# Kernel tuning notes

Measured on AMD Instinct MI355X. Metric: run time of the kernel, lower is better.

Reference implementation:

```python
import jax, jax.numpy as jnp
import numpy as np

B, S, HID = 1, 2048, 2048
H, KV, D = 32, 8, 64          # num_heads, num_kv_heads, head_dim
N_REP = H // KV               # GQA groups = 4
FF = 8192
EPS = 1e-5
ROPE_THETA = 10000.0


def _rope_tables(seq_len, dim, dtype=jnp.float32):
    inv_freq = 1.0 / (ROPE_THETA ** (jnp.arange(0, dim, 2, dtype=jnp.float32) / dim))
    t = jnp.arange(seq_len, dtype=jnp.float32)
    freqs = jnp.outer(t, inv_freq)                 # [S, D/2]
    emb = jnp.concatenate([freqs, freqs], axis=-1) # [S, D]
    return jnp.cos(emb).astype(dtype)[None], jnp.sin(emb).astype(dtype)[None]  # [1,S,D]


def setup_inputs() -> dict:
    key = jax.random.key(0)
    ks = jax.random.split(key, 10)
    s = 0.02
    cos, sin = _rope_tables(S, D)
    return {
        "hidden_states": jax.random.normal(ks[0], (B, S, HID), jnp.float32),
        "cos": cos, "sin": sin,
        "wq": jax.random.normal(ks[1], (HID, H * D), jnp.float32) * s,
        "wk": jax.random.normal(ks[2], (HID, KV * D), jnp.float32) * s,
        "wv": jax.random.normal(ks[3], (HID, KV * D), jnp.float32) * s,
        "wo": jax.random.normal(ks[4], (H * D, HID), jnp.float32) * s,
        "w_ln1": jnp.ones((HID,), jnp.float32),
        "w_ln2": jnp.ones((HID,), jnp.float32),
        "w_gate": jax.random.normal(ks[5], (HID, FF), jnp.float32) * s,
        "w_up": jax.random.normal(ks[6], (HID, FF), jnp.float32) * s,
        "w_down": jax.random.normal(ks[7], (FF, HID), jnp.float32) * s,
    }


def _rmsnorm(x, w):
    var = jnp.mean(jnp.square(x), axis=-1, keepdims=True)
    return x * jax.lax.rsqrt(var + EPS) * w


def _rotate_half(x):
    x1, x2 = jnp.split(x, 2, axis=-1)
    return jnp.concatenate([-x2, x1], axis=-1)


def _apply_rope(q, k, cos, sin):
    # q,k: [B,H,S,D]; cos,sin: [B,S,D] -> unsqueeze head dim
    c, s = cos[:, None], sin[:, None]
    return q * c + _rotate_half(q) * s, k * c + _rotate_half(k) * s


def reference(hidden_states, cos, sin, wq, wk, wv, wo, w_ln1, w_ln2, w_gate, w_up, w_down):
    residual = hidden_states
    x = _rmsnorm(hidden_states, w_ln1)

    q = (x @ wq).reshape(B, S, H, D).transpose(0, 2, 1, 3)    # [B,H,S,D]
    k = (x @ wk).reshape(B, S, KV, D).transpose(0, 2, 1, 3)   # [B,KV,S,D]
    v = (x @ wv).reshape(B, S, KV, D).transpose(0, 2, 1, 3)
    q, k = _apply_rope(q, k, cos, sin)

    # repeat_kv (interleaved) for GQA
    k = jnp.repeat(k, N_REP, axis=1)                           # [B,H,S,D]
    v = jnp.repeat(v, N_REP, axis=1)

    scale = 1.0 / np.sqrt(D)
    scores = jnp.einsum("bhqd,bhkd->bhqk", q, k) * scale       # [B,H,S,S]
    causal = jnp.tril(jnp.ones((S, S), bool))
    scores = jnp.where(causal, scores, jnp.finfo(scores.dtype).min)
    probs = jax.nn.softmax(scores, axis=-1)
    attn = jnp.einsum("bhqk,bhkd->bhqd", probs, v)             # [B,H,S,D]
    attn = attn.transpose(0, 2, 1, 3).reshape(B, S, H * D)
    attn = attn @ wo

    h = residual + attn
    residual = h
    y = _rmsnorm(h, w_ln2)
    mlp = (jax.nn.silu(y @ w_gate) * (y @ w_up)) @ w_down
    return residual + mlp
```

## Files before the change

kernel.cpp:

```cpp
#include <hip/hip_runtime.h>
#include <hip/hip_bf16.h>
#include <cstdint>

#define S_LEN 2048
#define HIDN  2048
#define NH    32
#define NKV   8
#define HD    64
#define FFN   8192
#define QKVN  3072
#define QKVLD 3072

typedef __attribute__((ext_vector_type(4)))  float f32x4;
typedef __attribute__((ext_vector_type(16))) float f32x16;
typedef __attribute__((ext_vector_type(8)))  short short8;
typedef __attribute__((ext_vector_type(4)))  short s16x4;

__device__ __forceinline__ short f2bf(float f) {
  union { float f; uint32_t u; } v; v.f = f;
  uint32_t r = v.u + 0x7FFFu + ((v.u >> 16) & 1u);
  return (short)(r >> 16);
}
__device__ __forceinline__ float bf2f(short s) {
  union { float f; uint32_t u; } v; v.u = ((uint32_t)(uint16_t)s) << 16;
  return v.f;
}
__device__ __forceinline__ unsigned packbf2(float lo, float hi) {
  return (unsigned)(uint16_t)f2bf(lo) | ((unsigned)(uint16_t)f2bf(hi) << 16);
}

#define GLOAD_LDS16(gp, lp) \
  __builtin_amdgcn_global_load_lds((const __attribute__((address_space(1))) void*)(gp), \
                                   (__attribute__((address_space(3))) void*)(lp), 16, 0, 0)

#define BARRIER()  asm volatile("s_barrier" ::: "memory")
#define LGKM0()    asm volatile("s_waitcnt lgkmcnt(0)" ::: "memory")
#define SCHED0()   __builtin_amdgcn_sched_barrier(0)
#define VMCNT(N)   asm volatile("s_waitcnt vmcnt(%0)" :: "n"(N) : "memory")

__global__ __launch_bounds__(256) void convT_kernel(const float* __restrict__ src,
    short* __restrict__ dst, int K, int N) {
  __shared__ float t[64][65];
  const int k0 = blockIdx.x * 64, n0 = blockIdx.y * 64;
  const int tr = threadIdx.x >> 4, tc = (threadIdx.x & 15) * 4;
  #pragma unroll
  for (int i = 0; i < 4; ++i) {
    float4 v = *(const float4*)(src + (size_t)(k0 + tr + i * 16) * N + n0 + tc);
    t[tr + i * 16][tc] = v.x; t[tr + i * 16][tc + 1] = v.y;
    t[tr + i * 16][tc + 2] = v.z; t[tr + i * 16][tc + 3] = v.w;
  }
  __syncthreads();
  const int dr = threadIdx.x >> 2, dc = (threadIdx.x & 3) * 16;
  short8 o0, o1;
  #pragma unroll
  for (int j = 0; j < 8; ++j) { o0[j] = f2bf(t[dc + j][dr]); o1[j] = f2bf(t[dc + 8 + j][dr]); }
  short* dp = dst + (size_t)(n0 + dr) * K + k0 + dc;
  *(short8*)dp = o0;
  *(short8*)(dp + 8) = o1;
}

__global__ __launch_bounds__(256) void convT_pack2_kernel(const float* __restrict__ wg,
    const float* __restrict__ wu, short* __restrict__ dst) {
  __shared__ float t[64][65];
  const int plane = blockIdx.z;
  const float* src = plane ? wu : wg;
  const int k0 = blockIdx.x * 64, n0 = blockIdx.y * 64;
  const int tr = threadIdx.x >> 4, tc = (threadIdx.x & 15) * 4;
  #pragma unroll
  for (int i = 0; i < 4; ++i) {
    float4 v = *(const float4*)(src + (size_t)(k0 + tr + i * 16) * FFN + n0 + tc);
    t[tr + i * 16][tc] = v.x; t[tr + i * 16][tc + 1] = v.y;
    t[tr + i * 16][tc + 2] = v.z; t[tr + i * 16][tc + 3] = v.w;
  }
  __syncthreads();
  const int dr = threadIdx.x >> 2, dc = (threadIdx.x & 3) * 16;
  const int n = n0 + dr;
  const int rr = ((n >> 4) << 5) + plane * 16 + (n & 15);
  short8 o0, o1;
  #pragma unroll
  for (int j = 0; j < 8; ++j) { o0[j] = f2bf(t[dc + j][dr]); o1[j] = f2bf(t[dc + 8 + j][dr]); }
  short* dp = dst + (size_t)rr * HIDN + k0 + dc;
  *(short8*)dp = o0;
  *(short8*)(dp + 8) = o1;
}

__global__ __launch_bounds__(256) void rmsnorm_kernel(const float* __restrict__ X,
    const float* __restrict__ W, short* __restrict__ Y) {
  int row = blockIdx.x;
  const float4* x4 = (const float4*)(X + (size_t)row * HIDN);
  const float4* w4 = (const float4*)W;
  float4 v0 = x4[2 * threadIdx.x];
  float4 v1 = x4[2 * threadIdx.x + 1];
  float ss = v0.x*v0.x + v0.y*v0.y + v0.z*v0.z + v0.w*v0.w
           + v1.x*v1.x + v1.y*v1.y + v1.z*v1.z + v1.w*v1.w;
  #pragma unroll
  for (int off = 32; off > 0; off >>= 1) ss += __shfl_xor(ss, off, 64);
  __shared__ float red[4];
  if ((threadIdx.x & 63) == 0) red[threadIdx.x >> 6] = ss;
  __syncthreads();
  ss = red[0] + red[1] + red[2] + red[3];
  float rs = rsqrtf(ss * (1.0f / HIDN) + 1e-5f);
  float4 w0 = w4[2 * threadIdx.x], w1 = w4[2 * threadIdx.x + 1];
  short8 o;
  o[0] = f2bf(v0.x * rs * w0.x); o[1] = f2bf(v0.y * rs * w0.y);
  o[2] = f2bf(v0.z * rs * w0.z); o[3] = f2bf(v0.w * rs * w0.w);
  o[4] = f2bf(v1.x * rs * w1.x); o[5] = f2bf(v1.y * rs * w1.y);
  o[6] = f2bf(v1.z * rs * w1.z); o[7] = f2bf(v1.w * rs * w1.w);
  *(short8*)(Y + (size_t)row * HIDN + threadIdx.x * 8) = o;
}

template<int EPI, int BN>
__global__ __launch_bounds__(512, 1) void gemm8p(const short* __restrict__ A,
    const short* __restrict__ BT, void* __restrict__ Cp, const void* __restrict__ Xp,
    int N, int Kfull, int KC, int gy) {
  constexpr int NFN = BN / 64;
  constexpr int LB  = BN / 128;
  constexpr int VN  = 2 + 2 * LB;
  __shared__ __align__(16) short As[2][256 * 64];
  __shared__ __align__(16) short Bs[2][BN * 64];
  const int tid = threadIdx.x, lane = tid & 63, w = tid >> 6;
  const int wm2 = w >> 2;
  const int wn = (w & 3) * (BN / 4);
  const int l15 = lane & 15, lg = lane >> 4;
  const int cpx = gy >> 3;
  const int xcd = blockIdx.x & 7, cid = blockIdx.x >> 3;
  const int by = xcd * cpx + cid % cpx, bx = cid / cpx;
  const int brow = bx * 256, bcol = by * BN;
  const size_t kbase = (size_t)blockIdx.z * KC;
  const int r8 = lane >> 3, c8 = lane & 7;
  const int gblk = c8 ^ r8;
  const int nt = KC / 64;
  f32x4 acc[8][NFN] = {};
  short8 af[4], bf[2][NFN];

  auto STA = [&](int p, int kt, int h) {
    const size_t kc = kbase + (size_t)kt * 64 + gblk * 8;
    #pragma unroll
    for (int j = 0; j < 2; ++j) {
      const short* g = A + (size_t)(brow + h * 128 + j * 64 + w * 8 + r8) * Kfull + kc;
      GLOAD_LDS16(g, &As[p][(h * 128 + j * 64 + w * 8) * 64]);
    }
  };
  auto STB = [&](int p, int kt, int h) {
    const size_t kc = kbase + (size_t)kt * 64 + gblk * 8;
    #pragma unroll
    for (int j = 0; j < LB; ++j) {
      const short* g = BT + (size_t)(bcol + h * (BN / 2) + j * 64 + w * 8 + r8) * Kfull + kc;
      GLOAD_LDS16(g, &Bs[p][(h * (BN / 2) + j * 64 + w * 8) * 64]);
    }
  };
  auto LDA = [&](int p, int mh, int kk) {
    #pragma unroll
    for (int m = 0; m < 4; ++m) {
      const int row = mh * 128 + wm2 * 64 + m * 16 + l15;
      af[m] = *(const short8*)&As[p][row * 64 + (((kk * 4 + lg) ^ (row & 7)) * 8)];
    }
  };
  auto LDB = [&](int p, int kk) {
    #pragma unroll
    for (int n = 0; n < NFN; ++n) {
      const int row = wn + n * 16 + l15;
      bf[kk][n] = *(const short8*)&Bs[p][row * 64 + (((kk * 4 + lg) ^ (row & 7)) * 8)];
    }
  };

#define MMQ(MH, KK) \
  __builtin_amdgcn_s_setprio(1); \
  _Pragma("unroll") \
  for (int m = 0; m < 4; ++m) \
    _Pragma("unroll") \
    for (int n = 0; n < NFN; ++n) \
      acc[(MH) * 4 + m][n] = __builtin_amdgcn_mfma_f32_16x16x32_bf16(af[m], bf[KK][n], acc[(MH) * 4 + m][n], 0, 0, 0); \
  __builtin_amdgcn_s_setprio(0);

  STB(0, 0, 0); STB(0, 0, 1); STA(0, 0, 0); STA(0, 0, 1);
  STB(1, 1, 0); STB(1, 1, 1); STA(1, 1, 0);
  VMCNT(VN);
  BARRIER();

  for (int i = 0; i < nt / 2; ++i) {
    const int t = 2 * i;
    const bool li = (i == nt / 2 - 1);
    LDA(0, 0, 0); LDB(0, 0); LDB(0, 1);
    STA(1, t + 1, 1);
    BARRIER(); LGKM0(); SCHED0();
    MMQ(0, 0);
    BARRIER();
    LDA(0, 0, 1);
    if (!li) STB(0, t + 2, 0);
    BARRIER(); LGKM0(); SCHED0();
    MMQ(0, 1);
    BARRIER();
    LDA(0, 1, 0);
    if (!li) STB(0, t + 2, 1);
    BARRIER(); LGKM0(); SCHED0();
    MMQ(1, 0);
    BARRIER();
    LDA(0, 1, 1);
    if (!li) STA(0, t + 2, 0);
    BARRIER(); LGKM0(); SCHED0();
    MMQ(1, 1);
    if (li) { VMCNT(0); } else { VMCNT(VN); }
    BARRIER();
    LDA(1, 0, 0); LDB(1, 0); LDB(1, 1);
    if (!li) STA(0, t + 2, 1);
    BARRIER(); LGKM0(); SCHED0();
    MMQ(0, 0);
    BARRIER();
    LDA(1, 0, 1);
    if (!li) STB(1, t + 3, 0);
    BARRIER(); LGKM0(); SCHED0();
    MMQ(0, 1);
    BARRIER();
    LDA(1, 1, 0);
    if (!li) STB(1, t + 3, 1);
    BARRIER(); LGKM0(); SCHED0();
    MMQ(1, 0);
    BARRIER();
    LDA(1, 1, 1);
    if (!li) STA(1, t + 3, 0);
    BARRIER(); LGKM0(); SCHED0();
    MMQ(1, 1);
    if (!li) { VMCNT(VN); }
    BARRIER();
  }
#undef MMQ

  if (EPI == 4) {
    const int No = N >> 1;
    const bool evn = (l15 & 1) == 0;
    #pragma unroll
    for (int mf = 0; mf < 8; ++mf) {
      const int r0 = brow + (mf >> 2) * 128 + wm2 * 64 + (mf & 3) * 16 + lg * 4;
      #pragma unroll
      for (int jg = 0; jg < NFN / 2; ++jg) {
        const int c = (bcol >> 1) + (wn >> 1) + jg * 16 + l15;
        #pragma unroll
        for (int i4 = 0; i4 < 4; ++i4) {
          float gt = acc[mf][2 * jg][i4];
          float up = acc[mf][2 * jg + 1][i4];
          float r = gt / (1.f + __expf(-gt)) * up;
          float ro = __shfl_xor(r, 1);
          if (evn)
            *(unsigned*)((short*)Cp + (size_t)(r0 + i4) * No + c) = packbf2(r, ro);
        }
      }
    }
  } else {
    #pragma unroll
    for (int mf = 0; mf < 8; ++mf) {
      const int r0 = brow + (mf >> 2) * 128 + wm2 * 64 + (mf & 3) * 16 + lg * 4;
      #pragma unroll
      for (int nf = 0; nf < NFN; ++nf) {
        const int c = bcol + wn + nf * 16 + l15;
        #pragma unroll
        for (int i4 = 0; i4 < 4; ++i4) {
          const size_t idx = (size_t)(r0 + i4) * N + c;
          float v = acc[mf][nf][i4];
          if (EPI == 0) ((short*)Cp)[idx] = f2bf(v);
          if (EPI == 1) ((float*)Cp)[idx] = v + ((const float*)Xp)[idx];
          if (EPI == 5) ((short*)Cp)[(size_t)blockIdx.z * S_LEN * N + idx] = f2bf(v);
        }
      }
    }
  }
}

__global__ __launch_bounds__(256) void rope_kernel(short* __restrict__ qkv,
    const float* __restrict__ cosb, const float* __restrict__ sinb) {
  int idx = blockIdx.x * 256 + threadIdx.x;
  int d = idx & 31;
  int hh = (idx >> 5) % (NH + NKV);
  int s = idx / (32 * (NH + NKV));
  int col = (hh < NH) ? hh * HD : HIDN + (hh - NH) * HD;
  short* base = qkv + (size_t)s * QKVLD + col;
  float c  = cosb[s * HD + d];
  float sn = sinb[s * HD + d];
  float x1 = bf2f(base[d]), x2 = bf2f(base[d + 32]);
  base[d]      = f2bf(x1 * c - x2 * sn);
  base[d + 32] = f2bf(x2 * c + x1 * sn);
}

__global__ __launch_bounds__(256) void attn_kernel(const short* __restrict__ QKV,
    short* __restrict__ O) {
  __shared__ __align__(16) short Ks[64][72];
  __shared__ __align__(16) short VTs[64][72];
  const int bid = blockIdx.x;
  const int half = bid >> 8, idx = bid & 255;
  const int h = idx & 31;
  int qt = idx >> 5;
  qt = half ? (15 - qt) : qt;
  const int kvh = h >> 2;
  const int tid = threadIdx.x, lane = tid & 63, w = tid >> 6;
  const int l31 = lane & 31, hi = lane >> 5;
  const int qb = qt * 128 + w * 32;
  const int kcol = HIDN + kvh * HD;
  const int vcol = HIDN + NKV * HD + kvh * HD;

  short8 Qr[4];
  {
    const short* qp = QKV + (size_t)(qb + l31) * QKVLD + h * HD;
    #pragma unroll
    for (int dk = 0; dk < 4; ++dk) {
      short8 qv = *(const short8*)(qp + dk * 16 + hi * 8);
      #pragma unroll
      for (int e = 0; e < 8; ++e) Qr[dk][e] = f2bf(bf2f(qv[e]) * 0.125f);
    }
  }
  float m_ = -3e38f, l_ = 0.f;
  f32x16 o0 = {}, o1 = {};
  const int nt = 2 * qt + 2;
  const int krow = tid >> 2, kcb = (tid & 3) * 16;
  const int vk = tid & 31, vdb = (tid >> 5) * 8;

  short8 kr0, kr1, vr0, vr1;
  {
    const short* gk = QKV + (size_t)krow * QKVLD + kcol + kcb;
    kr0 = *(const short8*)gk; kr1 = *(const short8*)(gk + 8);
    vr0 = *(const short8*)(QKV + (size_t)vk * QKVLD + vcol + vdb);
    vr1 = *(const short8*)(QKV + (size_t)(32 + vk) * QKVLD + vcol + vdb);
  }

  for (int t = 0; t < nt; ++t) {
    const int kb = t * 64;
    BARRIER();
    *(short8*)&Ks[krow][kcb] = kr0;
    *(short8*)&Ks[krow][kcb + 8] = kr1;
    #pragma unroll
    for (int j = 0; j < 8; ++j) VTs[vdb + j][vk] = vr0[j];
    #pragma unroll
    for (int j = 0; j < 8; ++j) VTs[vdb + j][32 + vk] = vr1[j];
    LGKM0();
    BARRIER();
    if (t + 1 < nt) {
      const int kb2 = kb + 64;
      const short* gk = QKV + (size_t)(kb2 + krow) * QKVLD + kcol + kcb;
      kr0 = *(const short8*)gk; kr1 = *(const short8*)(gk + 8);
      vr0 = *(const short8*)(QKV + (size_t)(kb2 + vk) * QKVLD + vcol + vdb);
      vr1 = *(const short8*)(QKV + (size_t)(kb2 + 32 + vk) * QKVLD + vcol + vdb);
    }
    if (kb < qb + 32) {
      f32x16 s[2] = {};
      __builtin_amdgcn_s_setprio(1);
      #pragma unroll
      for (int kt = 0; kt < 2; ++kt)
        #pragma unroll
        for (int dk = 0; dk < 4; ++dk) {
          short8 kf = *(const short8*)&Ks[kt * 32 + l31][dk * 16 + hi * 8];
          s[kt] = __builtin_amdgcn_mfma_f32_32x32x16_bf16(kf, Qr[dk], s[kt], 0, 0, 0);
        }
      __builtin_amdgcn_s_setprio(0);
      if (kb + 63 > qb) {
        const int qg = qb + l31;
        #pragma unroll
        for (int kt = 0; kt < 2; ++kt)
          #pragma unroll
          for (int r = 0; r < 16; ++r) {
            const int kg = kb + kt * 32 + (r & 3) + 8 * (r >> 2) + 4 * hi;
            if (kg > qg) s[kt][r] = -1e30f;
          }
      }
      float pm = s[0][0];
      #pragma unroll
      for (int r = 1; r < 16; ++r) pm = fmaxf(pm, s[0][r]);
      #pragma unroll
      for (int r = 0; r < 16; ++r) pm = fmaxf(pm, s[1][r]);
      pm = fmaxf(pm, __shfl_xor(pm, 32));
      const float mn = fmaxf(m_, pm);
      const float al = __expf(m_ - mn);
      float rsum = 0.f;
      #pragma unroll
      for (int kt = 0; kt < 2; ++kt)
        #pragma unroll
        for (int r = 0; r < 16; ++r) { s[kt][r] = __expf(s[kt][r] - mn); rsum += s[kt][r]; }
      rsum += __shfl_xor(rsum, 32);
      l_ = l_ * al + rsum;
      m_ = mn;
      o0 *= al; o1 *= al;
      unsigned wd[2][8], rw[2][8];
      #pragma unroll
      for (int kt = 0; kt < 2; ++kt)
        #pragma unroll
        for (int i = 0; i < 8; ++i) {
          wd[kt][i] = packbf2(s[kt][2 * i], s[kt][2 * i + 1]);
          rw[kt][i] = (unsigned)__shfl_xor((int)wd[kt][i], 32);
        }
      #pragma unroll
      for (int kt = 0; kt < 2; ++kt) {
        union { unsigned u[4]; short8 s8; } pf0, pf1;
        if (hi) {
          pf0.u[0] = rw[kt][2]; pf0.u[1] = rw[kt][3]; pf0.u[2] = wd[kt][2]; pf0.u[3] = wd[kt][3];
          pf1.u[0] = rw[kt][6]; pf1.u[1] = rw[kt][7]; pf1.u[2] = wd[kt][6]; pf1.u[3] = wd[kt][7];
        } else {
          pf0.u[0] = wd[kt][0]; pf0.u[1] = wd[kt][1]; pf0.u[2] = rw[kt][0]; pf0.u[3] = rw[kt][1];
          pf1.u[0] = wd[kt][4]; pf1.u[1] = wd[kt][5]; pf1.u[2] = rw[kt][4]; pf1.u[3] = rw[kt][5];
        }
        __builtin_amdgcn_s_setprio(1);
        #pragma unroll
        for (int ks = 0; ks < 2; ++ks) {
          const short8 pB = ks ? pf1.s8 : pf0.s8;
          short8 va = *(const short8*)&VTs[l31][kt * 32 + ks * 16 + hi * 8];
          o0 = __builtin_amdgcn_mfma_f32_32x32x16_bf16(va, pB, o0, 0, 0, 0);
          short8 vb = *(const short8*)&VTs[32 + l31][kt * 32 + ks * 16 + hi * 8];
          o1 = __builtin_amdgcn_mfma_f32_32x32x16_bf16(vb, pB, o1, 0, 0, 0);
        }
        __builtin_amdgcn_s_setprio(0);
      }
    }
  }
  const float inv = 1.f / l_;
  short* op = O + (size_t)(qb + l31) * HIDN + h * HD;
  #pragma unroll
  for (int dt = 0; dt < 2; ++dt) {
    const f32x16& o = dt ? o1 : o0;
    #pragma unroll
    for (int g = 0; g < 4; ++g) {
      s16x4 st;
      st[0] = f2bf(o[g * 4 + 0] * inv);
      st[1] = f2bf(o[g * 4 + 1] * inv);
      st[2] = f2bf(o[g * 4 + 2] * inv);
      st[3] = f2bf(o[g * 4 + 3] * inv);
      *(s16x4*)(op + dt * 32 + g * 8 + hi * 4) = st;
    }
  }
}

__global__ __launch_bounds__(256) void reduce4_kernel(float* __restrict__ out,
    const short* __restrict__ P) {
  const size_t n = (size_t)S_LEN * HIDN;
  size_t i = ((size_t)blockIdx.x * 256 + threadIdx.x) * 4;
  float4 o = *(float4*)(out + i);
  float s0 = 0.f, s1 = 0.f, s2 = 0.f, s3 = 0.f;
  #pragma unroll
  for (int z = 0; z < 4; ++z) {
    s16x4 p = *(const s16x4*)(P + z * n + i);
    s0 += bf2f(p[0]); s1 += bf2f(p[1]); s2 += bf2f(p[2]); s3 += bf2f(p[3]);
  }
  o.x += s0; o.y += s1; o.z += s2; o.w += s3;
  *(float4*)(out + i) = o;
}

extern "C" void kernel_launch(void* const* d_in, const int* in_sizes, int n_in,
                              void* d_out, int out_size, void* d_ws, size_t ws_size,
                              hipStream_t stream) {
  const float* hs   = (const float*)d_in[0];
  const float* cosb = (const float*)d_in[1];
  const float* sinb = (const float*)d_in[2];
  const float* wq   = (const float*)d_in[3];
  const float* wk   = (const float*)d_in[4];
  const float* wv   = (const float*)d_in[5];
  const float* wo   = (const float*)d_in[6];
  const float* wln1 = (const float*)d_in[7];
  const float* wln2 = (const float*)d_in[8];
  const float* wg   = (const float*)d_in[9];
  const float* wu   = (const float*)d_in[10];
  const float* wd   = (const float*)d_in[11];
  float* out = (float*)d_out;
  char* ws = (char*)d_ws;
  const size_t MB = 1024 * 1024;
  short* Wbig  = (short*)(ws);
  short* Wqkv  = Wbig;
  short* xn    = (short*)(ws + 13 * MB);
  short* qkv   = (short*)(ws + 21 * MB);
  short* attnO = (short*)(ws + 34 * MB);
  short* Wwo   = (short*)(ws + 42 * MB);
  short* y     = (short*)(ws + 64 * MB);
  short* g     = (short*)(ws + 72 * MB);
  short* Wd    = Wbig;
  short* P     = (short*)(ws + 32 * MB);

  convT_kernel<<<dim3(32, 32), 256, 0, stream>>>(wq, Wqkv, HIDN, NH * HD);
  convT_kernel<<<dim3(32, 8),  256, 0, stream>>>(wk, Wqkv + (size_t)2048 * HIDN, HIDN, NKV * HD);
  convT_kernel<<<dim3(32, 8),  256, 0, stream>>>(wv, Wqkv + (size_t)2560 * HIDN, HIDN, NKV * HD);
  rmsnorm_kernel<<<S_LEN, 256, 0, stream>>>(hs, wln1, xn);
  gemm8p<0, 128><<<dim3(192, 1, 1), 512, 0, stream>>>(xn, Wqkv, qkv, nullptr, QKVN, HIDN, HIDN, 24);
  convT_kernel<<<dim3(32, 32), 256, 0, stream>>>(wo, Wwo, NH * HD, HIDN);
  rope_kernel<<<(S_LEN * (NH + NKV) * 32) / 256, 256, 0, stream>>>(qkv, cosb, sinb);
  attn_kernel<<<NH * (S_LEN / 128), 256, 0, stream>>>(qkv, attnO);
  gemm8p<1, 128><<<dim3(128, 1, 1), 512, 0, stream>>>(attnO, Wwo, out, hs, HIDN, NH * HD, NH * HD, 16);
  rmsnorm_kernel<<<S_LEN, 256, 0, stream>>>(out, wln2, y);
  convT_pack2_kernel<<<dim3(32, 128, 2), 256, 0, stream>>>(wg, wu, Wbig);
  gemm8p<4, 256><<<dim3(512, 1, 1), 512, 0, stream>>>(y, Wbig, g, nullptr, 2 * FFN, HIDN, HIDN, 64);
  convT_kernel<<<dim3(128, 32), 256, 0, stream>>>(wd, Wd, FFN, HIDN);
  gemm8p<5, 256><<<dim3(64, 1, 4), 512, 0, stream>>>(g, Wd, P, nullptr, HIDN, FFN, FFN / 4, 8);
  reduce4_kernel<<<(S_LEN * HIDN) / 1024, 256, 0, stream>>>(out, P);
}
```

Baseline: 434.1 us.

## Fuse Q RoPE into attention, enlarge KV tiles, split-K Wo with fused norm

Q-side RoPE now happens inside the attention kernel's Q load, so the standalone rope kernel only rotates K. The attention loop stages 128-key tiles per barrier instead of 64, halving the number of synchronisation rounds at the cost of more LDS. The Wo projection becomes a two-way split-K GEMM writing bf16 partials. A new kernel sums those partials with the residual and applies the second RMSNorm in one pass, replacing the separate fp32 epilogue and rmsnorm launch. The SwiGLU epilogue drops the shuffle-and-pack store for plain per-element bf16 stores, and the split-K partials add bf16 rounding.

```diff
diff --git a/kernel.cpp b/kernel.cpp
--- a/kernel.cpp
+++ b/kernel.cpp
@@ -107,6 +107,48 @@
   o[4] = f2bf(v1.x * rs * w1.x); o[5] = f2bf(v1.y * rs * w1.y);
   o[6] = f2bf(v1.z * rs * w1.z); o[7] = f2bf(v1.w * rs * w1.w);
   *(short8*)(Y + (size_t)row * HIDN + threadIdx.x * 8) = o;
+}
+
+__global__ __launch_bounds__(256) void wo_norm_kernel(float* __restrict__ out,
+    const float* __restrict__ hs, const short* __restrict__ P,
+    const float* __restrict__ W, short* __restrict__ Y) {
+  const size_t n = (size_t)S_LEN * HIDN;
+  const int row = blockIdx.x;
+  const size_t base = (size_t)row * HIDN + threadIdx.x * 8;
+  float4 h0 = *(const float4*)(hs + base);
+  float4 h1 = *(const float4*)(hs + base + 4);
+  short8 a = *(const short8*)(P + base);
+  short8 b = *(const short8*)(P + n + base);
+  float v[8];
+  v[0] = h0.x + bf2f(a[0]) + bf2f(b[0]);
+  v[1] = h0.y + bf2f(a[1]) + bf2f(b[1]);
+  v[2] = h0.z + bf2f(a[2]) + bf2f(b[2]);
+  v[3] = h0.w + bf2f(a[3]) + bf2f(b[3]);
+  v[4] = h1.x + bf2f(a[4]) + bf2f(b[4]);
+  v[5] = h1.y + bf2f(a[5]) + bf2f(b[5]);
+  v[6] = h1.z + bf2f(a[6]) + bf2f(b[6]);
+  v[7] = h1.w + bf2f(a[7]) + bf2f(b[7]);
+  float4 o0 = {v[0], v[1], v[2], v[3]}, o1 = {v[4], v[5], v[6], v[7]};
+  *(float4*)(out + base) = o0;
+  *(float4*)(out + base + 4) = o1;
+  float ss = 0.f;
+  #pragma unroll
+  for (int j = 0; j < 8; ++j) ss += v[j] * v[j];
+  #pragma unroll
+  for (int off = 32; off > 0; off >>= 1) ss += __shfl_xor(ss, off, 64);
+  __shared__ float red[4];
+  if ((threadIdx.x & 63) == 0) red[threadIdx.x >> 6] = ss;
+  __syncthreads();
+  ss = red[0] + red[1] + red[2] + red[3];
+  float rs = rsqrtf(ss * (1.0f / HIDN) + 1e-5f);
+  float4 w0 = *(const float4*)(W + threadIdx.x * 8);
+  float4 w1 = *(const float4*)(W + threadIdx.x * 8 + 4);
+  short8 o;
+  o[0] = f2bf(v[0] * rs * w0.x); o[1] = f2bf(v[1] * rs * w0.y);
+  o[2] = f2bf(v[2] * rs * w0.z); o[3] = f2bf(v[3] * rs * w0.w);
+  o[4] = f2bf(v[4] * rs * w1.x); o[5] = f2bf(v[5] * rs * w1.y);
+  o[6] = f2bf(v[6] * rs * w1.z); o[7] = f2bf(v[7] * rs * w1.w);
+  *(short8*)(Y + base) = o;
 }
 
 template<int EPI, int BN>
@@ -228,7 +270,6 @@
 
   if (EPI == 4) {
     const int No = N >> 1;
-    const bool evn = (l15 & 1) == 0;
     #pragma unroll
     for (int mf = 0; mf < 8; ++mf) {
       const int r0 = brow + (mf >> 2) * 128 + wm2 * 64 + (mf & 3) * 16 + lg * 4;
@@ -239,10 +280,7 @@
         for (int i4 = 0; i4 < 4; ++i4) {
           float gt = acc[mf][2 * jg][i4];
           float up = acc[mf][2 * jg + 1][i4];
-          float r = gt / (1.f + __expf(-gt)) * up;
-          float ro = __shfl_xor(r, 1);
-          if (evn)
-            *(unsigned*)((short*)Cp + (size_t)(r0 + i4) * No + c) = packbf2(r, ro);
+          ((short*)Cp)[(size_t)(r0 + i4) * No + c] = f2bf(gt / (1.f + __expf(-gt)) * up);
         }
       }
     }
@@ -266,14 +304,13 @@
   }
 }
 
-__global__ __launch_bounds__(256) void rope_kernel(short* __restrict__ qkv,
+__global__ __launch_bounds__(256) void rope_k_kernel(short* __restrict__ qkv,
     const float* __restrict__ cosb, const float* __restrict__ sinb) {
   int idx = blockIdx.x * 256 + threadIdx.x;
   int d = idx & 31;
-  int hh = (idx >> 5) % (NH + NKV);
-  int s = idx / (32 * (NH + NKV));
-  int col = (hh < NH) ? hh * HD : HIDN + (hh - NH) * HD;
-  short* base = qkv + (size_t)s * QKVLD + col;
+  int hh = (idx >> 5) & (NKV - 1);
+  int s = idx >> 8;
+  short* base = qkv + (size_t)s * QKVLD + HIDN + hh * HD;
   float c  = cosb[s * HD + d];
   float sn = sinb[s * HD + d];
   float x1 = bf2f(base[d]), x2 = bf2f(base[d + 32]);
@@ -282,14 +319,15 @@
 }
 
 __global__ __launch_bounds__(256) void attn_kernel(const short* __restrict__ QKV,
+    const float* __restrict__ cosb, const float* __restrict__ sinb,
     short* __restrict__ O) {
-  __shared__ __align__(16) short Ks[64][72];
-  __shared__ __align__(16) short VTs[64][72];
+  __shared__ __align__(16) short Ks[128][72];
+  __shared__ __align__(16) short VTs[64][136];
   const int bid = blockIdx.x;
-  const int half = bid >> 8, idx = bid & 255;
+  const int half_ = bid >> 8, idx = bid & 255;
   const int h = idx & 31;
   int qt = idx >> 5;
-  qt = half ? (15 - qt) : qt;
+  qt = half_ ? (15 - qt) : qt;
   const int kvh = h >> 2;
   const int tid = threadIdx.x, lane = tid & 63, w = tid >> 6;
   const int l31 = lane & 31, hi = lane >> 5;
@@ -299,112 +337,135 @@
 
   short8 Qr[4];
   {
-    const short* qp = QKV + (size_t)(qb + l31) * QKVLD + h * HD;
-    #pragma unroll
-    for (int dk = 0; dk < 4; ++dk) {
-      short8 qv = *(const short8*)(qp + dk * 16 + hi * 8);
-      #pragma unroll
-      for (int e = 0; e < 8; ++e) Qr[dk][e] = f2bf(bf2f(qv[e]) * 0.125f);
-    }
+    const int s = qb + l31;
+    const short* qp = QKV + (size_t)s * QKVLD + h * HD;
+    short8 qv[4];
+    #pragma unroll
+    for (int dk = 0; dk < 4; ++dk) qv[dk] = *(const short8*)(qp + dk * 16 + hi * 8);
+    const float* cp = cosb + s * HD;
+    const float* sp = sinb + s * HD;
+    #pragma unroll
+    for (int dk = 0; dk < 2; ++dk)
+      #pragma unroll
+      for (int e = 0; e < 8; ++e) {
+        const int d = dk * 16 + hi * 8 + e;
+        float c = cp[d], sn = sp[d];
+        float x1 = bf2f(qv[dk][e]), x2 = bf2f(qv[dk + 2][e]);
+        Qr[dk][e]     = f2bf((x1 * c - x2 * sn) * 0.125f);
+        Qr[dk + 2][e] = f2bf((x2 * c + x1 * sn) * 0.125f);
+      }
   }
   float m_ = -3e38f, l_ = 0.f;
   f32x16 o0 = {}, o1 = {};
-  const int nt = 2 * qt + 2;
-  const int krow = tid >> 2, kcb = (tid & 3) * 16;
-  const int vk = tid & 31, vdb = (tid >> 5) * 8;
-
-  short8 kr0, kr1, vr0, vr1;
+  const int nt = qt + 1;
+  const int kr_ = tid >> 1, kdb = (tid & 1) * 32;
+
+  short8 kr0, kr1, kr2, kr3, vr0, vr1, vr2, vr3;
   {
-    const short* gk = QKV + (size_t)krow * QKVLD + kcol + kcb;
-    kr0 = *(const short8*)gk; kr1 = *(const short8*)(gk + 8);
-    vr0 = *(const short8*)(QKV + (size_t)vk * QKVLD + vcol + vdb);
-    vr1 = *(const short8*)(QKV + (size_t)(32 + vk) * QKVLD + vcol + vdb);
+    const short* gk = QKV + (size_t)kr_ * QKVLD + kcol + kdb;
+    kr0 = *(const short8*)gk;        kr1 = *(const short8*)(gk + 8);
+    kr2 = *(const short8*)(gk + 16); kr3 = *(const short8*)(gk + 24);
+    const short* gv = QKV + (size_t)kr_ * QKVLD + vcol + kdb;
+    vr0 = *(const short8*)gv;        vr1 = *(const short8*)(gv + 8);
+    vr2 = *(const short8*)(gv + 16); vr3 = *(const short8*)(gv + 24);
   }
 
   for (int t = 0; t < nt; ++t) {
-    const int kb = t * 64;
-    BARRIER();
-    *(short8*)&Ks[krow][kcb] = kr0;
-    *(short8*)&Ks[krow][kcb + 8] = kr1;
-    #pragma unroll
-    for (int j = 0; j < 8; ++j) VTs[vdb + j][vk] = vr0[j];
-    #pragma unroll
-    for (int j = 0; j < 8; ++j) VTs[vdb + j][32 + vk] = vr1[j];
+    const int kb = t * 128;
+    BARRIER();
+    {
+      short8* kp = (short8*)&Ks[kr_][kdb];
+      kp[0] = kr0; kp[1] = kr1; kp[2] = kr2; kp[3] = kr3;
+      #pragma unroll
+      for (int j = 0; j < 8; ++j) VTs[kdb + j][kr_]      = vr0[j];
+      #pragma unroll
+      for (int j = 0; j < 8; ++j) VTs[kdb + 8 + j][kr_]  = vr1[j];
+      #pragma unroll
+      for (int j = 0; j < 8; ++j) VTs[kdb + 16 + j][kr_] = vr2[j];
+      #pragma unroll
+      for (int j = 0; j < 8; ++j) VTs[kdb + 24 + j][kr_] = vr3[j];
+    }
     LGKM0();
     BARRIER();
     if (t + 1 < nt) {
-      const int kb2 = kb + 64;
-      const short* gk = QKV + (size_t)(kb2 + krow) * QKVLD + kcol + kcb;
-      kr0 = *(const short8*)gk; kr1 = *(const short8*)(gk + 8);
-      vr0 = *(const short8*)(QKV + (size_t)(kb2 + vk) * QKVLD + vcol + vdb);
-      vr1 = *(const short8*)(QKV + (size_t)(kb2 + 32 + vk) * QKVLD + vcol + vdb);
-    }
-    if (kb < qb + 32) {
-      f32x16 s[2] = {};
-      __builtin_amdgcn_s_setprio(1);
-      #pragma unroll
-      for (int kt = 0; kt < 2; ++kt)
-        #pragma unroll
-        for (int dk = 0; dk < 4; ++dk) {
-          short8 kf = *(const short8*)&Ks[kt * 32 + l31][dk * 16 + hi * 8];
-          s[kt] = __builtin_amdgcn_mfma_f32_32x32x16_bf16(kf, Qr[dk], s[kt], 0, 0, 0);
-        }
-      __builtin_amdgcn_s_setprio(0);
-      if (kb + 63 > qb) {
-        const int qg = qb + l31;
+      const int kb2 = kb + 128;
+      const short* gk = QKV + (size_t)(kb2 + kr_) * QKVLD + kcol + kdb;
+      kr0 = *(const short8*)gk;        kr1 = *(const short8*)(gk + 8);
+      kr2 = *(const short8*)(gk + 16); kr3 = *(const short8*)(gk + 24);
+      const short* gv = QKV + (size_t)(kb2 + kr_) * QKVLD + vcol + kdb;
+      vr0 = *(const short8*)gv;        vr1 = *(const short8*)(gv + 8);
+      vr2 = *(const short8*)(gv + 16); vr3 = *(const short8*)(gv + 24);
+    }
+    #pragma unroll
+    for (int hf = 0; hf < 2; ++hf) {
+      const int hb = kb + hf * 64;
+      if (hb < qb + 32) {
+        f32x16 s[2] = {};
+        __builtin_amdgcn_s_setprio(1);
         #pragma unroll
         for (int kt = 0; kt < 2; ++kt)
           #pragma unroll
-          for (int r = 0; r < 16; ++r) {
-            const int kg = kb + kt * 32 + (r & 3) + 8 * (r >> 2) + 4 * hi;
-            if (kg > qg) s[kt][r] = -1e30f;
+          for (int dk = 0; dk < 4; ++dk) {
+            short8 kf = *(const short8*)&Ks[hf * 64 + kt * 32 + l31][dk * 16 + hi * 8];
+            s[kt] = __builtin_amdgcn_mfma_f32_32x32x16_bf16(kf, Qr[dk], s[kt], 0, 0, 0);
           }
-      }
-      float pm = s[0][0];
-      #pragma unroll
-      for (int r = 1; r < 16; ++r) pm = fmaxf(pm, s[0][r]);
-      #pragma unroll
-      for (int r = 0; r < 16; ++r) pm = fmaxf(pm, s[1][r]);
-      pm = fmaxf(pm, __shfl_xor(pm, 32));
-      const float mn = fmaxf(m_, pm);
-      const float al = __expf(m_ - mn);
-      float rsum = 0.f;
-      #pragma unroll
-      for (int kt = 0; kt < 2; ++kt)
-        #pragma unroll
-        for (int r = 0; r < 16; ++r) { s[kt][r] = __expf(s[kt][r] - mn); rsum += s[kt][r]; }
-      rsum += __shfl_xor(rsum, 32);
-      l_ = l_ * al + rsum;
-      m_ = mn;
-      o0 *= al; o1 *= al;
-      unsigned wd[2][8], rw[2][8];
-      #pragma unroll
-      for (int kt = 0; kt < 2; ++kt)
-        #pragma unroll
-        for (int i = 0; i < 8; ++i) {
-          wd[kt][i] = packbf2(s[kt][2 * i], s[kt][2 * i + 1]);
-          rw[kt][i] = (unsigned)__shfl_xor((int)wd[kt][i], 32);
+        __builtin_amdgcn_s_setprio(0);
+        if (hb + 63 > qb) {
+          const int qg = qb + l31;
+          #pragma unroll
+          for (int kt = 0; kt < 2; ++kt)
+            #pragma unroll
+            for (int r = 0; r < 16; ++r) {
+              const int kg = hb + kt * 32 + (r & 3) + 8 * (r >> 2) + 4 * hi;
+              if (kg > qg) s[kt][r] = -1e30f;
+            }
         }
-      #pragma unroll
-      for (int kt = 0; kt < 2; ++kt) {
-        union { unsigned u[4]; short8 s8; } pf0, pf1;
-        if (hi) {
-          pf0.u[0] = rw[kt][2]; pf0.u[1] = rw[kt][3]; pf0.u[2] = wd[kt][2]; pf0.u[3] = wd[kt][3];
-          pf1.u[0] = rw[kt][6]; pf1.u[1] = rw[kt][7]; pf1.u[2] = wd[kt][6]; pf1.u[3] = wd[kt][7];
-        } else {
-          pf0.u[0] = wd[kt][0]; pf0.u[1] = wd[kt][1]; pf0.u[2] = rw[kt][0]; pf0.u[3] = rw[kt][1];
-          pf1.u[0] = wd[kt][4]; pf1.u[1] = wd[kt][5]; pf1.u[2] = rw[kt][4]; pf1.u[3] = rw[kt][5];
+        float pm = s[0][0];
+        #pragma unroll
+        for (int r = 1; r < 16; ++r) pm = fmaxf(pm, s[0][r]);
+        #pragma unroll
+        for (int r = 0; r < 16; ++r) pm = fmaxf(pm, s[1][r]);
+        pm = fmaxf(pm, __shfl_xor(pm, 32));
+        const float mn = fmaxf(m_, pm);
+        const float al = __expf(m_ - mn);
+        float rsum = 0.f;
+        #pragma unroll
+        for (int kt = 0; kt < 2; ++kt)
+          #pragma unroll
+          for (int r = 0; r < 16; ++r) { s[kt][r] = __expf(s[kt][r] - mn); rsum += s[kt][r]; }
+        rsum += __shfl_xor(rsum, 32);
+        l_ = l_ * al + rsum;
+        m_ = mn;
+        o0 *= al; o1 *= al;
+        unsigned wd[2][8], rw[2][8];
+        #pragma unroll
+        for (int kt = 0; kt < 2; ++kt)
+          #pragma unroll
+          for (int i = 0; i < 8; ++i) {
+            wd[kt][i] = packbf2(s[kt][2 * i], s[kt][2 * i + 1]);
+            rw[kt][i] = (unsigned)__shfl_xor((int)wd[kt][i], 32);
+          }
+        #pragma unroll
+        for (int kt = 0; kt < 2; ++kt) {
+          union { unsigned u[4]; short8 s8; } pf0, pf1;
+          if (hi) {
+            pf0.u[0] = rw[kt][2]; pf0.u[1] = rw[kt][3]; pf0.u[2] = wd[kt][2]; pf0.u[3] = wd[kt][3];
+            pf1.u[0] = rw[kt][6]; pf1.u[1] = rw[kt][7]; pf1.u[2] = wd[kt][6]; pf1.u[3] = wd[kt][7];
+          } else {
+            pf0.u[0] = wd[kt][0]; pf0.u[1] = wd[kt][1]; pf0.u[2] = rw[kt][0]; pf0.u[3] = rw[kt][1];
+            pf1.u[0] = wd[kt][4]; pf1.u[1] = wd[kt][5]; pf1.u[2] = rw[kt][4]; pf1.u[3] = rw[kt][5];
+          }
+          __builtin_amdgcn_s_setprio(1);
+          #pragma unroll
+          for (int ks = 0; ks < 2; ++ks) {
+            const short8 pB = ks ? pf1.s8 : pf0.s8;
+            short8 va = *(const short8*)&VTs[l31][hf * 64 + kt * 32 + ks * 16 + hi * 8];
+            o0 = __builtin_amdgcn_mfma_f32_32x32x16_bf16(va, pB, o0, 0, 0, 0);
+            short8 vb = *(const short8*)&VTs[32 + l31][hf * 64 + kt * 32 + ks * 16 + hi * 8];
+            o1 = __builtin_amdgcn_mfma_f32_32x32x16_bf16(vb, pB, o1, 0, 0, 0);
+          }
+          __builtin_amdgcn_s_setprio(0);
         }
-        __builtin_amdgcn_s_setprio(1);
-        #pragma unroll
-        for (int ks = 0; ks < 2; ++ks) {
-          const short8 pB = ks ? pf1.s8 : pf0.s8;
-          short8 va = *(const short8*)&VTs[l31][kt * 32 + ks * 16 + hi * 8];
-          o0 = __builtin_amdgcn_mfma_f32_32x32x16_bf16(va, pB, o0, 0, 0, 0);
-          short8 vb = *(const short8*)&VTs[32 + l31][kt * 32 + ks * 16 + hi * 8];
-          o1 = __builtin_amdgcn_mfma_f32_32x32x16_bf16(vb, pB, o1, 0, 0, 0);
-        }
-        __builtin_amdgcn_s_setprio(0);
       }
     }
   }
@@ -464,6 +525,7 @@
   short* qkv   = (short*)(ws + 21 * MB);
   short* attnO = (short*)(ws + 34 * MB);
   short* Wwo   = (short*)(ws + 42 * MB);
+  short* Pwo   = (short*)(ws);
   short* y     = (short*)(ws + 64 * MB);
   short* g     = (short*)(ws + 72 * MB);
   short* Wd    = Wbig;
@@ -475,10 +537,10 @@
   rmsnorm_kernel<<<S_LEN, 256, 0, stream>>>(hs, wln1, xn);
   gemm8p<0, 128><<<dim3(192, 1, 1), 512, 0, stream>>>(xn, Wqkv, qkv, nullptr, QKVN, HIDN, HIDN, 24);
   convT_kernel<<<dim3(32, 32), 256, 0, stream>>>(wo, Wwo, NH * HD, HIDN);
-  rope_kernel<<<(S_LEN * (NH + NKV) * 32) / 256, 256, 0, stream>>>(qkv, cosb, sinb);
-  attn_kernel<<<NH * (S_LEN / 128), 256, 0, stream>>>(qkv, attnO);
-  gemm8p<1, 128><<<dim3(128, 1, 1), 512, 0, stream>>>(attnO, Wwo, out, hs, HIDN, NH * HD, NH * HD, 16);
-  rmsnorm_kernel<<<S_LEN, 256, 0, stream>>>(out, wln2, y);
+  rope_k_kernel<<<(S_LEN * NKV * 32) / 256, 256, 0, stream>>>(qkv, cosb, sinb);
+  attn_kernel<<<NH * (S_LEN / 128), 256, 0, stream>>>(qkv, cosb, sinb, attnO);
+  gemm8p<5, 128><<<dim3(128, 1, 2), 512, 0, stream>>>(attnO, Wwo, Pwo, nullptr, HIDN, NH * HD, NH * HD / 2, 16);
+  wo_norm_kernel<<<S_LEN, 256, 0, stream>>>(out, hs, Pwo, wln2, y);
   convT_pack2_kernel<<<dim3(32, 128, 2), 256, 0, stream>>>(wg, wu, Wbig);
   gemm8p<4, 256><<<dim3(512, 1, 1), 512, 0, stream>>>(y, Wbig, g, nullptr, 2 * FFN, HIDN, HIDN, 64);
   convT_kernel<<<dim3(128, 32), 256, 0, stream>>>(wd, Wd, FFN, HIDN);
```

After: 408.7 us. -5.9%, faster.
